# Kernel tuning notes

Measured on AMD Instinct MI355X. Metric: run time of the kernel, lower is better.

The kernel has to match this reference:

```python
import jax, jax.numpy as jnp
import numpy as np

PY_SIZES = [256, 64]
BASE = 256


def _resize_bilinear_ac(x, out):
    # NCHW bilinear resize, align_corners=True (matches F.interpolate(..., align_corners=True))
    def interp(x, axis, in_size):
        pos = jnp.arange(out, dtype=jnp.float32) * (in_size - 1) / (out - 1)
        lo = jnp.floor(pos).astype(jnp.int32)
        hi = jnp.minimum(lo + 1, in_size - 1)
        w = (pos - lo.astype(jnp.float32)).astype(x.dtype)
        shp = [1] * x.ndim
        shp[axis] = out
        w = w.reshape(shp)
        return jnp.take(x, lo, axis=axis) * (1 - w) + jnp.take(x, hi, axis=axis) * w
    x = interp(x, 2, x.shape[2])
    x = interp(x, 3, x.shape[3])
    return x


def _area_pool(x, f):
    # F.interpolate(mode='area') for integer downscale factor f == average pooling
    B, C, H, W = x.shape
    return x.reshape(B, C, H // f, f, W // f, f).mean(axis=(3, 5))


def _nearest_up_int(x, out):
    # F.interpolate(mode='nearest'): src = floor(dst * in/out)
    h = x.shape[2]
    idx = (jnp.arange(out) * h) // out
    return x[:, :, idx][:, :, :, idx]


def _buffers(B):
    grids, lin_ids, img_ids = [], [], []
    prev = 0
    for S in PY_SIZES:
        d = jnp.arange(S, dtype=jnp.float32) + 0.5
        gy, gx = jnp.meshgrid(d, d, indexing='ij')
        grids.append(jnp.broadcast_to(jnp.stack([gy, gx], -1)[None, None], (B, 1, S, S, 2)))
        lin_ids.append(jnp.arange(B * S * S, dtype=jnp.int32).reshape(B, 1, S, S) + prev)
        prev += B * S * S
        img_ids.append(jnp.broadcast_to(jnp.arange(B, dtype=jnp.float32)[:, None, None, None], (B, 1, S, S)))
    return grids, lin_ids, img_ids


def setup_inputs():
    key = jax.random.key(0)
    k1, k2 = jax.random.split(key)
    b_edges = (jax.random.uniform(k1, (64, 1, 512, 512)) < 0.08).astype(jnp.float32)
    sobel = jax.random.normal(k2, (64, 2, 512, 512), dtype=jnp.float32)
    return {"b_edges": b_edges, "sobel": sobel}


def reference(b_edges, sobel):
    B = b_edges.shape[0]
    grids, lin_ids, img_ids = _buffers(B)
    # resize post-Canny maps to base pyramid level
    e0 = jnp.clip(_resize_bilinear_ac(b_edges, BASE), 0, 1)
    s0 = _resize_bilinear_ac(sobel, BASE)
    py = [(e0, s0)]
    for S in PY_SIZES[1:]:
        f = BASE // S
        py.append((_area_pool(e0, f), _area_pool(s0, f)))
    p_lin, my_lin, centers, norms, sizes, imgid = [], [], [], [], [], []
    for i, (e, s) in enumerate(py):
        S = e.shape[2]
        idx = jnp.nonzero((e != 0).reshape(-1))[0]  # stream compaction of edge pixels
        if i + 1 < len(py):
            pl = _nearest_up_int(lin_ids[i + 1], S).reshape(-1)[idx]
        else:
            pl = lin_ids[i].reshape(-1)[idx]
        rat = BASE / S
        p_lin.append(pl)
        my_lin.append(lin_ids[i].reshape(-1)[idx])
        centers.append(grids[i].reshape(-1, 2)[idx] * rat)
        norms.append(jnp.transpose(s, (0, 2, 3, 1)).reshape(-1, 2)[idx])
        sizes.append(jnp.full(idx.shape, rat, dtype=jnp.float32))
        imgid.append(img_ids[i].reshape(-1)[idx])
    p_lin = jnp.concatenate(p_lin)
    my_lin = jnp.concatenate(my_lin)
    centers = jnp.concatenate(centers)
    norms = jnp.concatenate(norms)
    sizes = jnp.concatenate(sizes)
    imgid = jnp.concatenate(imgid)
    # parent scatter: linid -> row of that string, then gather by parent linid
    rowids = jnp.arange(my_lin.shape[0], dtype=jnp.int32)
    table = jnp.zeros(int(p_lin.max()) + 1, dtype=jnp.int32).at[my_lin].set(rowids)
    p_rowids = table[p_lin]
    norms = norms / jnp.linalg.norm(norms, axis=1, keepdims=True)
    # cross([nx,ny,0],[0,0,1]) = (ny,-nx,0)
    rt = jnp.stack([norms[:, 1], -norms[:, 0]], -1) * (sizes[:, None] / 2)
    locs_lf = centers + rt
    locs_rt = centers - rt
    return locs_lf, locs_rt, norms, sizes, centers, imgid, p_rowids, my_lin
```

## Files before the change

### kernel.cpp

```cpp
#include <hip/hip_runtime.h>
#include <math.h>


typedef unsigned long long u64;
#define OFFSET1 4194304

__global__ __launch_bounds__(256) void prepE_kernel(const float* __restrict__ E,
                                                    unsigned short* __restrict__ pred16,
                                                    u64* __restrict__ mask1,
                                                    int* __restrict__ counts0,
                                                    int* __restrict__ counts1) {
    int lane = threadIdx.x & 63;
    int g = blockIdx.x * 4 + (threadIdx.x >> 6);
    int b = g >> 6, R = g & 63;

    const float* Ep = E + b * 262144 + (8 * R) * 512 + 8 * lane;
    float4 L[8], H[8];
    #pragma unroll
    for (int k = 0; k < 8; ++k) {
        L[k] = *(const float4*)(Ep + k * 512);
        H[k] = *(const float4*)(Ep + k * 512 + 4);
    }

    float wx[4], cwx[4];
    #pragma unroll
    for (int j = 0; j < 4; ++j) {
        int xi = 4 * lane + j;
        wx[j] = (float)(xi * 511) / 255.0f - (float)(8 * lane + 2 * j);
        cwx[j] = 1.0f - wx[j];
    }

    unsigned pred = 0;
    int rc = 0;
    #pragma unroll
    for (int r = 0; r < 4; ++r) {
        int y = 4 * R + r;
        float wy = (float)(y * 511) / 255.0f - (float)(2 * y);
        float cwy = 1.0f - wy;
        float4 lo = L[2 * r], loh = H[2 * r];
        float4 hi = L[2 * r + 1], hih = H[2 * r + 1];
        float e0 = (lo.x*cwy + hi.x*wy)*cwx[0] + (lo.y*cwy + hi.y*wy)*wx[0];
        float e1 = (lo.z*cwy + hi.z*wy)*cwx[1] + (lo.w*cwy + hi.w*wy)*wx[1];
        float e2 = (loh.x*cwy + hih.x*wy)*cwx[2] + (loh.y*cwy + hih.y*wy)*wx[2];
        float e3 = (loh.z*cwy + hih.z*wy)*cwx[3] + (loh.w*cwy + hih.w*wy)*wx[3];
        bool p0 = (e0 != 0.0f), p1 = (e1 != 0.0f), p2 = (e2 != 0.0f), p3 = (e3 != 0.0f);
        pred |= (p0?1u:0u) << (4*r+0);
        pred |= (p1?1u:0u) << (4*r+1);
        pred |= (p2?1u:0u) << (4*r+2);
        pred |= (p3?1u:0u) << (4*r+3);
        u64 b0 = __ballot(p0), b1 = __ballot(p1), b2 = __ballot(p2), b3 = __ballot(p3);
        rc += __popcll(b0) + __popcll(b1) + __popcll(b2) + __popcll(b3);
    }
    u64 m1 = __ballot(pred != 0);
    pred16[g * 64 + lane] = (unsigned short)pred;
    if (lane == 0) {
        counts0[g] = rc;
        counts1[g] = __popcll(m1);
        mask1[g] = m1;
    }
}

__global__ __launch_bounds__(1024) void scan_kernel(const int* __restrict__ counts0,
                                                    int* __restrict__ offs0,
                                                    const int* __restrict__ counts1,
                                                    int* __restrict__ offs1,
                                                    int* __restrict__ totals) {
    __shared__ int wsum[16];
    int tid = threadIdx.x, lane = tid & 63, wave = tid >> 6;

    int carry = 0;
    for (int base = 0; base < 4096; base += 1024) {
        int v = counts0[base + tid];
        int inc = v;
        #pragma unroll
        for (int d = 1; d < 64; d <<= 1) {
            int t = __shfl_up(inc, (unsigned)d, 64);
            if (lane >= d) inc += t;
        }
        if (lane == 63) wsum[wave] = inc;
        __syncthreads();
        int wbase = 0;
        for (int i = 0; i < wave; ++i) wbase += wsum[i];
        int tot = 0;
        #pragma unroll
        for (int i = 0; i < 16; ++i) tot += wsum[i];
        offs0[base + tid] = carry + wbase + inc - v;
        carry += tot;
        __syncthreads();
    }
    if (tid == 0) totals[0] = carry;

    int carry1 = 0;
    for (int base = 0; base < 4096; base += 1024) {
        int v = counts1[base + tid];
        int inc = v;
        #pragma unroll
        for (int d = 1; d < 64; d <<= 1) {
            int t = __shfl_up(inc, (unsigned)d, 64);
            if (lane >= d) inc += t;
        }
        if (lane == 63) wsum[wave] = inc;
        __syncthreads();
        int wbase = 0;
        for (int i = 0; i < wave; ++i) wbase += wsum[i];
        int tot = 0;
        #pragma unroll
        for (int i = 0; i < 16; ++i) tot += wsum[i];
        offs1[base + tid] = carry1 + wbase + inc - v;
        carry1 += tot;
        __syncthreads();
    }
    if (tid == 0) totals[1] = carry1;
}

__device__ __forceinline__ void write_row(float* __restrict__ out, int N, int row,
                                          float cy, float cx, float s0v, float s1v,
                                          float half, float sz, float imgid,
                                          float prow, float mylin) {
    float len = sqrtf(s0v * s0v + s1v * s1v);
    float n0 = s0v / len, n1 = s1v / len;
    float rt0 = n1 * half, rt1 = -n0 * half;
    ((float2*)out)[row]           = make_float2(cy + rt0, cx + rt1);
    ((float2*)(out + 2 * N))[row] = make_float2(cy - rt0, cx - rt1);
    ((float2*)(out + 4 * N))[row] = make_float2(n0, n1);
    out[6 * N + row] = sz;
    ((float2*)(out + 7 * N))[row] = make_float2(cy, cx);
    out[9 * N + row] = imgid;
    out[10 * N + row] = prow;
    out[11 * N + row] = mylin;
}

__global__ __launch_bounds__(256) void prepSa_kernel(const float* __restrict__ S,
                                                     const unsigned short* __restrict__ pred16,
                                                     const u64* __restrict__ mask1,
                                                     const int* __restrict__ offs0,
                                                     const int* __restrict__ offs1,
                                                     const int* __restrict__ totals,
                                                     float2* __restrict__ part,
                                                     float* __restrict__ out, int N) {
    int tid = threadIdx.x;
    int lane = tid & 63;
    int gh = blockIdx.x * 4 + (tid >> 6);
    int g = gh >> 1, h = gh & 1;
    int bimg = g >> 6, R = g & 63;

    unsigned pred = pred16[g * 64 + lane];
    u64 m1 = mask1[g];
    int base0 = offs0[g];
    int prow = totals[0] + offs1[g] + __popcll(m1 & ((1ull << lane) - 1ull));

    float wx[4], cwx[4];
    #pragma unroll
    for (int j = 0; j < 4; ++j) {
        int xi = 4 * lane + j;
        wx[j] = (float)(xi * 511) / 255.0f - (float)(8 * lane + 2 * j);
        cwx[j] = 1.0f - wx[j];
    }

    const float* Sa = S + (size_t)(2 * bimg) * 262144 + (8 * R + 4 * h) * 512 + 8 * lane;
    const float* Sq = Sa + 262144;
    float4 A[4], Ax[4], Q[4], Qx[4];
    #pragma unroll
    for (int k = 0; k < 4; ++k) {
        A[k]  = *(const float4*)(Sa + k * 512);
        Ax[k] = *(const float4*)(Sa + k * 512 + 4);
        Q[k]  = *(const float4*)(Sq + k * 512);
        Qx[k] = *(const float4*)(Sq + k * 512 + 4);
    }

    int rc = 0;
    if (h) {
        #pragma unroll
        for (int r = 0; r < 2; ++r) {
            unsigned pr = (pred >> (4 * r)) & 0xF;
            rc += __popcll(__ballot((pr & 1) != 0)) + __popcll(__ballot((pr & 2) != 0)) +
                  __popcll(__ballot((pr & 4) != 0)) + __popcll(__ballot((pr & 8) != 0));
        }
    }

    float acc0 = 0.0f, acc1 = 0.0f;
    #pragma unroll
    for (int rr = 0; rr < 2; ++rr) {
        int r = 2 * h + rr;
        int y = 4 * R + r;
        float wy = (float)(y * 511) / 255.0f - (float)(2 * y);
        float cwy = 1.0f - wy;
        float4 lo = A[2*rr], loh = Ax[2*rr], hi = A[2*rr+1], hih = Ax[2*rr+1];
        float4 ql = Q[2*rr], qlh = Qx[2*rr], qh = Q[2*rr+1], qhh = Qx[2*rr+1];
        float va[4], vb[4];
        va[0] = (lo.x*cwy + hi.x*wy)*cwx[0] + (lo.y*cwy + hi.y*wy)*wx[0];
        va[1] = (lo.z*cwy + hi.z*wy)*cwx[1] + (lo.w*cwy + hi.w*wy)*wx[1];
        va[2] = (loh.x*cwy + hih.x*wy)*cwx[2] + (loh.y*cwy + hih.y*wy)*wx[2];
        va[3] = (loh.z*cwy + hih.z*wy)*cwx[3] + (loh.w*cwy + hih.w*wy)*wx[3];
        vb[0] = (ql.x*cwy + qh.x*wy)*cwx[0] + (ql.y*cwy + qh.y*wy)*wx[0];
        vb[1] = (ql.z*cwy + qh.z*wy)*cwx[1] + (ql.w*cwy + qh.w*wy)*wx[1];
        vb[2] = (qlh.x*cwy + qhh.x*wy)*cwx[2] + (qlh.y*cwy + qhh.y*wy)*wx[2];
        vb[3] = (qlh.z*cwy + qhh.z*wy)*cwx[3] + (qlh.w*cwy + qhh.w*wy)*wx[3];
        acc0 += va[0] + va[1] + va[2] + va[3];
        acc1 += vb[0] + vb[1] + vb[2] + vb[3];

        unsigned pr = (pred >> (4 * r)) & 0xF;
        u64 b0 = __ballot((pr & 1) != 0);
        u64 b1 = __ballot((pr & 2) != 0);
        u64 b2 = __ballot((pr & 4) != 0);
        u64 b3 = __ballot((pr & 8) != 0);
        u64 ltm = (1ull << lane) - 1ull;
        int pre = __popcll(b0 & ltm) + __popcll(b1 & ltm) +
                  __popcll(b2 & ltm) + __popcll(b3 & ltm);
        int rbase = base0 + rc + pre;
        int own = 0;
        #pragma unroll
        for (int j = 0; j < 4; ++j) {
            if (pr & (1u << j)) {
                int row = rbase + own;
                own++;
                int x = 4 * lane + j;
                float cy = (float)y + 0.5f, cx = (float)x + 0.5f;
                write_row(out, N, row, cy, cx, va[j], vb[j], 0.5f, 1.0f,
                          (float)bimg, (float)prow,
                          (float)((bimg << 16) + (y << 8) + x));
            }
        }
        rc += __popcll(b0) + __popcll(b1) + __popcll(b2) + __popcll(b3);
    }

    part[gh * 64 + lane] = make_float2(acc0, acc1);
}

__global__ __launch_bounds__(256) void finish1_kernel(const float2* __restrict__ part,
                                                      const u64* __restrict__ mask1,
                                                      const int* __restrict__ offs1,
                                                      const int* __restrict__ totals,
                                                      float* __restrict__ out, int N) {
    int tid = threadIdx.x, lane = tid & 63;
    int g = blockIdx.x * 4 + (tid >> 6);
    u64 m1 = mask1[g];
    if (m1 == 0ull) return;
    float2 p0 = part[(2 * g) * 64 + lane];
    float2 p1 = part[(2 * g + 1) * 64 + lane];
    if (!((m1 >> lane) & 1ull)) return;
    int prow = totals[0] + offs1[g] + __popcll(m1 & ((1ull << lane) - 1ull));
    float v0 = (p0.x + p1.x) * (1.0f / 16.0f);
    float v1 = (p0.y + p1.y) * (1.0f / 16.0f);
    int bimg = g >> 6, R = g & 63;
    float cy = ((float)R + 0.5f) * 4.0f, cx = ((float)lane + 0.5f) * 4.0f;
    write_row(out, N, prow, cy, cx, v0, v1, 2.0f, 4.0f, (float)bimg,
              (float)prow, (float)(OFFSET1 + g * 64 + lane));
}

extern "C" void kernel_launch(void* const* d_in, const int* in_sizes, int n_in,
                              void* d_out, int out_size, void* d_ws, size_t ws_size,
                              hipStream_t stream) {
    const float* E = (const float*)d_in[0];
    const float* S = (const float*)d_in[1];
    float* out = (float*)d_out;
    int N = out_size / 12;

    char* ws = (char*)d_ws;
    int* counts0 = (int*)(ws + 0);
    int* offs0   = (int*)(ws + 16384);
    int* counts1 = (int*)(ws + 32768);
    int* offs1   = (int*)(ws + 49152);
    int* totals  = (int*)(ws + 65536);
    u64* mask1   = (u64*)(ws + 65600);
    unsigned short* pred16 = (unsigned short*)(ws + 98368);
    float2* part = (float2*)(ws + 622656);

    prepE_kernel<<<1024, 256, 0, stream>>>(E, pred16, mask1, counts0, counts1);
    scan_kernel<<<1, 1024, 0, stream>>>(counts0, offs0, counts1, offs1, totals);
    prepSa_kernel<<<2048, 256, 0, stream>>>(S, pred16, mask1, offs0, offs1,
                                            totals, part, out, N);
    finish1_kernel<<<1024, 256, 0, stream>>>(part, mask1, offs1, totals, out, N);
}
```

Baseline: 76.25 us.

## Stage output rows in LDS and write coalesced float4 section stores

Selected rows are no longer written straight to global memory from each lane in a scattered way. They are first staged into shared memory per block, using the scan offsets relative to the block's first row. After a barrier, each of the 8 output sections is written as a contiguous range with aligned float4 stores, and finish1 gets the same treatment. The aim is to replace many small, uncoalesced global writes with coalesced wide ones. This costs extra LDS use, a sync, recomputation of per-element values, sentinel scan entries and a reshuffled workspace layout.

```diff
diff --git a/kernel.cpp b/kernel.cpp
--- a/kernel.cpp
+++ b/kernel.cpp
@@ -88,7 +88,7 @@
         carry += tot;
         __syncthreads();
     }
-    if (tid == 0) totals[0] = carry;
+    if (tid == 0) { totals[0] = carry; offs0[4096] = carry; }
 
     int carry1 = 0;
     for (int base = 0; base < 4096; base += 1024) {
@@ -110,24 +110,74 @@
         carry1 += tot;
         __syncthreads();
     }
-    if (tid == 0) totals[1] = carry1;
-}
-
-__device__ __forceinline__ void write_row(float* __restrict__ out, int N, int row,
-                                          float cy, float cx, float s0v, float s1v,
-                                          float half, float sz, float imgid,
-                                          float prow, float mylin) {
-    float len = sqrtf(s0v * s0v + s1v * s1v);
-    float n0 = s0v / len, n1 = s1v / len;
+    if (tid == 0) { totals[1] = carry1; offs1[4096] = carry1; }
+}
+
+__device__ __forceinline__ float stage_val(int kind, int width, int f,
+                                           const float* lv0, const float* lv1,
+                                           const int* lpid, const int* lprw,
+                                           int level) {
+    int row = (width == 2) ? (f >> 1) : f;
+    int c   = (width == 2) ? (f & 1) : 0;
+    float v0 = lv0[row], v1 = lv1[row];
+    int pid = lpid[row], prw = lprw[row];
+    float cy, cx, half, sz, imgid, mylin;
+    if (level == 0) {
+        int b = pid >> 16, y = (pid >> 8) & 255, x = pid & 255;
+        cy = (float)y + 0.5f; cx = (float)x + 0.5f;
+        half = 0.5f; sz = 1.0f; imgid = (float)b; mylin = (float)pid;
+    } else {
+        int b = pid >> 12, R = (pid >> 6) & 63, X = pid & 63;
+        cy = ((float)R + 0.5f) * 4.0f; cx = ((float)X + 0.5f) * 4.0f;
+        half = 2.0f; sz = 4.0f; imgid = (float)b; mylin = (float)(OFFSET1 + pid);
+    }
+    float len = sqrtf(v0 * v0 + v1 * v1);
+    float n0 = v0 / len, n1 = v1 / len;
     float rt0 = n1 * half, rt1 = -n0 * half;
-    ((float2*)out)[row]           = make_float2(cy + rt0, cx + rt1);
-    ((float2*)(out + 2 * N))[row] = make_float2(cy - rt0, cx - rt1);
-    ((float2*)(out + 4 * N))[row] = make_float2(n0, n1);
-    out[6 * N + row] = sz;
-    ((float2*)(out + 7 * N))[row] = make_float2(cy, cx);
-    out[9 * N + row] = imgid;
-    out[10 * N + row] = prow;
-    out[11 * N + row] = mylin;
+    switch (kind) {
+        case 0: return c ? (cx + rt1) : (cy + rt0);
+        case 1: return c ? (cx - rt1) : (cy - rt0);
+        case 2: return c ? n1 : n0;
+        case 3: return sz;
+        case 4: return c ? cx : cy;
+        case 5: return imgid;
+        case 6: return (float)prw;
+        default: return mylin;
+    }
+}
+
+__device__ __forceinline__ void write_sections(float* __restrict__ out, int N,
+                                               int rowStart, int cnt, int level,
+                                               const float* lv0, const float* lv1,
+                                               const int* lpid, const int* lprw,
+                                               int tid) {
+    const int mult[8] = {0, 2, 4, 6, 7, 9, 10, 11};
+    const int wid[8]  = {2, 2, 2, 1, 2, 1, 1, 1};
+    #pragma unroll 1
+    for (int s = 0; s < 8; ++s) {
+        int width = wid[s];
+        float* P = out + (size_t)mult[s] * N + (size_t)width * rowStart;
+        int total = width * cnt;
+        int head = (int)((16 - ((uintptr_t)P & 15)) & 15) >> 2;
+        if (head > total) head = total;
+        if (tid < head)
+            P[tid] = stage_val(s, width, tid, lv0, lv1, lpid, lprw, level);
+        int nb4 = (total - head) >> 2;
+        #pragma unroll 1
+        for (int k = tid; k < nb4; k += 256) {
+            int f = head + 4 * k;
+            float4 v;
+            v.x = stage_val(s, width, f + 0, lv0, lv1, lpid, lprw, level);
+            v.y = stage_val(s, width, f + 1, lv0, lv1, lpid, lprw, level);
+            v.z = stage_val(s, width, f + 2, lv0, lv1, lpid, lprw, level);
+            v.w = stage_val(s, width, f + 3, lv0, lv1, lpid, lprw, level);
+            *(float4*)(P + f) = v;
+        }
+        int done = head + 4 * nb4;
+        int rem = total - done;
+        if (tid < rem)
+            P[done + tid] = stage_val(s, width, done + tid, lv0, lv1, lpid, lprw, level);
+    }
 }
 
 __global__ __launch_bounds__(256) void prepSa_kernel(const float* __restrict__ S,
@@ -138,11 +188,16 @@
                                                      const int* __restrict__ totals,
                                                      float2* __restrict__ part,
                                                      float* __restrict__ out, int N) {
+    __shared__ float lv0[1024], lv1[1024];
+    __shared__ int lpid[1024], lprw[1024];
+
     int tid = threadIdx.x;
     int lane = tid & 63;
     int gh = blockIdx.x * 4 + (tid >> 6);
     int g = gh >> 1, h = gh & 1;
     int bimg = g >> 6, R = g & 63;
+    int g0 = blockIdx.x * 2;
+    int rowStart = offs0[g0];
 
     unsigned pred = pred16[g * 64 + lane];
     u64 m1 = mask1[g];
@@ -214,17 +269,21 @@
             if (pr & (1u << j)) {
                 int row = rbase + own;
                 own++;
-                int x = 4 * lane + j;
-                float cy = (float)y + 0.5f, cx = (float)x + 0.5f;
-                write_row(out, N, row, cy, cx, va[j], vb[j], 0.5f, 1.0f,
-                          (float)bimg, (float)prow,
-                          (float)((bimg << 16) + (y << 8) + x));
+                int lr = row - rowStart;
+                lv0[lr] = va[j];
+                lv1[lr] = vb[j];
+                lpid[lr] = (bimg << 16) | (y << 8) | (4 * lane + j);
+                lprw[lr] = prow;
             }
         }
         rc += __popcll(b0) + __popcll(b1) + __popcll(b2) + __popcll(b3);
     }
 
     part[gh * 64 + lane] = make_float2(acc0, acc1);
+
+    __syncthreads();
+    int cnt = offs0[g0 + 2] - rowStart;
+    write_sections(out, N, rowStart, cnt, 0, lv0, lv1, lpid, lprw, tid);
 }
 
 __global__ __launch_bounds__(256) void finish1_kernel(const float2* __restrict__ part,
@@ -232,20 +291,27 @@
                                                       const int* __restrict__ offs1,
                                                       const int* __restrict__ totals,
                                                       float* __restrict__ out, int N) {
+    __shared__ float lv0[256], lv1[256];
+    __shared__ int lpid[256], lprw[256];
     int tid = threadIdx.x, lane = tid & 63;
     int g = blockIdx.x * 4 + (tid >> 6);
+    int g0 = blockIdx.x * 4;
+    int base1 = offs1[g0];
+    int N0 = totals[0];
+
     u64 m1 = mask1[g];
-    if (m1 == 0ull) return;
     float2 p0 = part[(2 * g) * 64 + lane];
     float2 p1 = part[(2 * g + 1) * 64 + lane];
-    if (!((m1 >> lane) & 1ull)) return;
-    int prow = totals[0] + offs1[g] + __popcll(m1 & ((1ull << lane) - 1ull));
-    float v0 = (p0.x + p1.x) * (1.0f / 16.0f);
-    float v1 = (p0.y + p1.y) * (1.0f / 16.0f);
-    int bimg = g >> 6, R = g & 63;
-    float cy = ((float)R + 0.5f) * 4.0f, cx = ((float)lane + 0.5f) * 4.0f;
-    write_row(out, N, prow, cy, cx, v0, v1, 2.0f, 4.0f, (float)bimg,
-              (float)prow, (float)(OFFSET1 + g * 64 + lane));
+    if ((m1 >> lane) & 1ull) {
+        int lr = (offs1[g] - base1) + __popcll(m1 & ((1ull << lane) - 1ull));
+        lv0[lr] = (p0.x + p1.x) * (1.0f / 16.0f);
+        lv1[lr] = (p0.y + p1.y) * (1.0f / 16.0f);
+        lpid[lr] = g * 64 + lane;
+        lprw[lr] = N0 + base1 + lr;
+    }
+    __syncthreads();
+    int cnt = offs1[g0 + 4] - base1;
+    write_sections(out, N, N0 + base1, cnt, 1, lv0, lv1, lpid, lprw, tid);
 }
 
 extern "C" void kernel_launch(void* const* d_in, const int* in_sizes, int n_in,
@@ -258,13 +324,13 @@
 
     char* ws = (char*)d_ws;
     int* counts0 = (int*)(ws + 0);
-    int* offs0   = (int*)(ws + 16384);
-    int* counts1 = (int*)(ws + 32768);
-    int* offs1   = (int*)(ws + 49152);
-    int* totals  = (int*)(ws + 65536);
-    u64* mask1   = (u64*)(ws + 65600);
-    unsigned short* pred16 = (unsigned short*)(ws + 98368);
-    float2* part = (float2*)(ws + 622656);
+    int* counts1 = (int*)(ws + 16384);
+    int* offs0   = (int*)(ws + 32768);
+    int* offs1   = (int*)(ws + 49216);
+    int* totals  = (int*)(ws + 65664);
+    u64* mask1   = (u64*)(ws + 65728);
+    unsigned short* pred16 = (unsigned short*)(ws + 98496);
+    float2* part = (float2*)(ws + 622784);
 
     prepE_kernel<<<1024, 256, 0, stream>>>(E, pred16, mask1, counts0, counts1);
     scan_kernel<<<1, 1024, 0, stream>>>(counts0, offs0, counts1, offs1, totals);
```

Result: slower. 88.72 us (+16.4%).
